# Optimization experiments

Hardware: AMD Instinct MI355X
Metric: run time of the kernel (lower is better)

## Reference

```python
import jax, jax.numpy as jnp
import numpy as np

FEAT_DIM = 1024
NUM_HEAD = 8


def setup_inputs() -> dict:
    key = jax.random.key(0)
    ks = jax.random.split(key, 8)
    D = FEAT_DIM
    s = D ** -0.5
    return {
        "motion": jax.random.normal(ks[0], (8, 1024, D), dtype=jnp.float32),
        "scene_feats": jax.random.normal(ks[1], (8, 2048, D), dtype=jnp.float32),
        # nn.Linear weights stored as [in, out] (already transposed for x @ W)
        "Wq": jax.random.normal(ks[2], (D, D), dtype=jnp.float32) * s,
        "bq": jax.random.normal(ks[3], (D,), dtype=jnp.float32) * s,
        "Wkv": jax.random.normal(ks[4], (D, 2 * D), dtype=jnp.float32) * s,
        "bkv": jax.random.normal(ks[5], (2 * D,), dtype=jnp.float32) * s,
        "Wout": jax.random.normal(ks[6], (D, D), dtype=jnp.float32) * s,
        "bout": jax.random.normal(ks[7], (D,), dtype=jnp.float32) * s,
    }


def reference(motion, scene_feats, Wq, bq, Wkv, bkv, Wout, bout):
    bs, L, D = motion.shape
    N = scene_feats.shape[1]
    H = NUM_HEAD
    Dh = D // H

    # q scaled by full feat_dim**-0.5 (as in source, not head_dim)
    q = (motion @ Wq + bq) * (D ** -0.5)
    kv = scene_feats @ Wkv + bkv
    k, v = kv[..., :D], kv[..., D:]

    # Faithful to source: q is viewed as (bs, H, L, Dh) with NO transpose,
    # while k, v use view(bs, N, H, Dh) followed by transpose(1, 2).
    q = q.reshape(bs, H, L, Dh)                      # [bs,H,L,Dh] (layout quirk)
    k = k.reshape(bs, N, H, Dh).transpose(0, 2, 1, 3)  # [bs,H,N,Dh]
    v = v.reshape(bs, N, H, Dh).transpose(0, 2, 1, 3)  # [bs,H,N,Dh]

    att = jnp.einsum("bhld,bhnd->bhln", q, k)        # [bs,H,L,N]
    att = jax.nn.softmax(att, axis=-1)
    out = jnp.einsum("bhln,bhnd->bhld", att, v)      # [bs,H,L,Dh]
    out = out.reshape(bs, L, D)                      # contiguous view, matches torch .view
    return out @ Wout + bout
```

## Files before the change

kernel.cpp:

```cpp
#include <hip/hip_runtime.h>

typedef __attribute__((ext_vector_type(8))) short bf16x8;
typedef __attribute__((ext_vector_type(4))) float f32x4;
typedef __attribute__((ext_vector_type(4))) float f32x4v;

#define MFMA16(a,b,c) __builtin_amdgcn_mfma_f32_16x16x32_bf16((a),(b),(c),0,0,0)

__device__ __forceinline__ short f2bf(float f){
  unsigned u = __builtin_bit_cast(unsigned, f);
  u += 0x7fffu + ((u >> 16) & 1u);
  return (short)(u >> 16);
}

__device__ __forceinline__ void gload16(const void* g, void* l){
  __builtin_amdgcn_global_load_lds((const __attribute__((address_space(1))) unsigned*)g,
                                   (__attribute__((address_space(3))) unsigned*)l,
                                   16, 0, 0);
}

__global__ __launch_bounds__(256) void k_f2bf(const float* __restrict__ in,
                                              short* __restrict__ out, int n8){
  int i = blockIdx.x * 256 + threadIdx.x;
  if (i >= n8) return;
  f32x4v a = ((const f32x4v*)in)[i*2];
  f32x4v b = ((const f32x4v*)in)[i*2+1];
  bf16x8 o;
  o[0]=f2bf(a[0]); o[1]=f2bf(a[1]); o[2]=f2bf(a[2]); o[3]=f2bf(a[3]);
  o[4]=f2bf(b[0]); o[5]=f2bf(b[1]); o[6]=f2bf(b[2]); o[7]=f2bf(b[3]);
  ((bf16x8*)out)[i] = o;
}

__global__ __launch_bounds__(256) void k_prep_wT(const float* __restrict__ W,
                                                 short* __restrict__ Wt, int K, int N){
  int i = blockIdx.x * 256 + threadIdx.x;
  int total = (K >> 3) * N;
  if (i >= total) return;
  int n  = i % N;
  int k0 = (i / N) << 3;
  bf16x8 o;
#pragma unroll
  for (int j = 0; j < 8; ++j) o[j] = f2bf(W[(size_t)(k0 + j) * N + n]);
  *(bf16x8*)&Wt[(size_t)n * K + k0] = o;
}

template<int MODE>
__global__ __launch_bounds__(256, 4) void k_gemm(
    const short* __restrict__ A, const short* __restrict__ Bt,
    const float* __restrict__ bias, float scale,
    void* __restrict__ out0, void* __restrict__ out1,
    int M, int N, int K)
{
  __shared__ __align__(16) short Alds[2][128 * 32];
  __shared__ __align__(16) short Blds[2][128 * 32];
  const int tid = threadIdx.x;
  const int l = tid & 63, w = tid >> 6;
  const int m0 = blockIdx.y * 128, n0 = blockIdx.x * 128;
  const int wr = w >> 1, wc = w & 1;
  const int lr = l & 15, lg = l >> 4;

  const int srow = l >> 2;
  const int scol = 8 * ((l & 3) ^ (srow & 3));
  const int acol = 8 * (lg ^ (lr & 3));

  f32x4 acc[4][4];
#pragma unroll
  for (int a = 0; a < 4; ++a)
#pragma unroll
    for (int b = 0; b < 4; ++b) acc[a][b] = (f32x4)(0.0f);

  const int nk = K >> 5;
  auto stage = [&](int kt, int buf){
    int k0 = kt << 5;
#pragma unroll
    for (int i = 0; i < 4; ++i){
      int c = w * 4 + i;
      if (c < 8){
        int m = c * 16 + srow;
        gload16(A + (size_t)(m0 + m) * K + k0 + scol, &Alds[buf][c * 512]);
      } else {
        int n = (c - 8) * 16 + srow;
        gload16(Bt + (size_t)(n0 + n) * K + k0 + scol, &Blds[buf][(c - 8) * 512]);
      }
    }
  };

  stage(0, 0);
  __syncthreads();
  int cur = 0;
  for (int kt = 0; kt < nk; ++kt){
    if (kt + 1 < nk) stage(kt + 1, cur ^ 1);
    bf16x8 af[4], bfv[4];
#pragma unroll
    for (int mi = 0; mi < 4; ++mi){
      int row = wr * 64 + mi * 16 + lr;
      af[mi] = *(const bf16x8*)&Alds[cur][row * 32 + acol];
    }
#pragma unroll
    for (int ni = 0; ni < 4; ++ni){
      int row = wc * 64 + ni * 16 + lr;
      bfv[ni] = *(const bf16x8*)&Blds[cur][row * 32 + acol];
    }
#pragma unroll
    for (int mi = 0; mi < 4; ++mi)
#pragma unroll
      for (int ni = 0; ni < 4; ++ni)
        acc[mi][ni] = MFMA16(af[mi], bfv[ni], acc[mi][ni]);
    __syncthreads();
    cur ^= 1;
  }

#pragma unroll
  for (int mi = 0; mi < 4; ++mi)
#pragma unroll
    for (int ni = 0; ni < 4; ++ni){
      int col = n0 + wc * 64 + ni * 16 + lr;
      float bv = bias[col];
#pragma unroll
      for (int r = 0; r < 4; ++r){
        int row = m0 + wr * 64 + mi * 16 + lg * 4 + r;
        float v = acc[mi][ni][r] + bv;
        if (MODE == 0){
          v *= scale;
          int b = row >> 10, lp = row & 1023;
          int h = lp >> 7;
          int lq = ((lp & 127) << 3) | (col >> 7);
          int dh = col & 127;
          ((short*)out0)[(((size_t)(b * 8 + h)) * 1024 + lq) * 128 + dh] = f2bf(v);
        } else if (MODE == 1){
          int b = row >> 11, nn = row & 2047;
          if (col < 1024){
            int h = col >> 7, dh = col & 127;
            ((short*)out0)[(((size_t)(b * 8 + h)) * 2048 + nn) * 128 + dh] = f2bf(v);
          } else {
            int c2 = col - 1024, h = c2 >> 7, dh = c2 & 127;
            ((short*)out1)[(((size_t)(b * 8 + h)) * 128 + dh) * 2048 + nn] = f2bf(v);
          }
        } else {
          ((float*)out0)[(size_t)row * N + col] = v;
        }
      }
    }
}

__global__ __launch_bounds__(512, 2) void k_attn(
    const short* __restrict__ Q, const short* __restrict__ K,
    const short* __restrict__ Vt, short* __restrict__ O)
{
  __shared__ __align__(16) short Klds[2][64 * 128];
  __shared__ __align__(16) short Vlds[2][128 * 64];
  __shared__ __align__(16) short Plds[8][32 * 64];
  const int tid = threadIdx.x;
  const int l = tid & 63, w = tid >> 6;
  const int lr = l & 15, lg = l >> 4;

  int flat = blockIdx.y * 4 + blockIdx.x;
  int xcd = flat & 7, idx = flat >> 3;
  int bh = xcd * 8 + (idx >> 2);
  int q0 = (idx & 3) * 256;

  const short* Qb = Q  + (size_t)bh * 1024 * 128;
  const short* Kb = K  + (size_t)bh * 2048 * 128;
  const short* Vb = Vt + (size_t)bh * 128 * 2048;

  bf16x8 qf[2][4];
#pragma unroll
  for (int mi = 0; mi < 2; ++mi)
#pragma unroll
    for (int kc = 0; kc < 4; ++kc)
      qf[mi][kc] = *(const bf16x8*)&Qb[(size_t)(q0 + w * 32 + mi * 16 + lr) * 128 + kc * 32 + lg * 8];

  f32x4 acc[8][2];
#pragma unroll
  for (int d = 0; d < 8; ++d){ acc[d][0] = (f32x4)(0.0f); acc[d][1] = (f32x4)(0.0f); }
  float mrun[2][4], lsum[2][4];
#pragma unroll
  for (int mi = 0; mi < 2; ++mi)
#pragma unroll
    for (int r = 0; r < 4; ++r){ mrun[mi][r] = -3e38f; lsum[mi][r] = 0.f; }

  auto stageK = [&](int t, int buf){
    int kv0 = t * 64;
#pragma unroll
    for (int i = 0; i < 2; ++i){
      int c = w * 2 + i;
      int row = 4 * c + (l >> 4);
      int col = ((l & 15) * 8) ^ ((row & 7) * 8);
      gload16(Kb + (size_t)(kv0 + row) * 128 + col, &Klds[buf][c * 512]);
    }
  };
  auto stageV = [&](int t, int buf){
    int kv0 = t * 64;
#pragma unroll
    for (int i = 0; i < 2; ++i){
      int c = w * 2 + i;
      int dh = 8 * c + (l >> 3);
      int col = ((l & 7) * 8) ^ (((l >> 3) & 7) * 8);
      gload16(Vb + (size_t)dh * 2048 + kv0 + col, &Vlds[buf][c * 512]);
    }
  };

  stageK(0, 0); stageV(0, 0);
  __syncthreads();
  int cur = 0;
  const int swz = (lr & 7) * 8;

  for (int t = 0; t < 32; ++t){
    if (t + 1 < 32){ stageK(t + 1, cur ^ 1); stageV(t + 1, cur ^ 1); }
    const short* Kl = &Klds[cur][0];
    const short* Vl = &Vlds[cur][0];
    short* Pw = &Plds[w][0];

    f32x4 s[2][4];
    __builtin_amdgcn_s_setprio(1);
#pragma unroll
    for (int nt = 0; nt < 4; ++nt){
      f32x4 s0 = (f32x4)(0.0f), s1 = (f32x4)(0.0f);
#pragma unroll
      for (int kc = 0; kc < 4; ++kc){
        bf16x8 kf = *(const bf16x8*)&Kl[(nt * 16 + lr) * 128 + ((kc * 32 + lg * 8) ^ swz)];
        s0 = MFMA16(qf[0][kc], kf, s0);
        s1 = MFMA16(qf[1][kc], kf, s1);
      }
      s[0][nt] = s0; s[1][nt] = s1;
    }
    __builtin_amdgcn_s_setprio(0);

    float pmax[2][4];
    int ok = 1;
#pragma unroll
    for (int mi = 0; mi < 2; ++mi)
#pragma unroll
      for (int r = 0; r < 4; ++r){
        float v = fmaxf(fmaxf(s[mi][0][r], s[mi][1][r]), fmaxf(s[mi][2][r], s[mi][3][r]));
        pmax[mi][r] = v;
        ok &= (v <= mrun[mi][r] + 8.0f) ? 1 : 0;
      }
    if (!__all(ok)){
#pragma unroll
      for (int mi = 0; mi < 2; ++mi)
#pragma unroll
        for (int r = 0; r < 4; ++r){
          float v = pmax[mi][r];
          v = fmaxf(v, __shfl_xor(v, 1, 16));
          v = fmaxf(v, __shfl_xor(v, 2, 16));
          v = fmaxf(v, __shfl_xor(v, 4, 16));
          v = fmaxf(v, __shfl_xor(v, 8, 16));
          float mnew = fmaxf(mrun[mi][r], v);
          float sc = exp2f(mrun[mi][r] - mnew);
          mrun[mi][r] = mnew;
          lsum[mi][r] *= sc;
#pragma unroll
          for (int d = 0; d < 8; ++d) acc[d][mi][r] *= sc;
        }
    }

#pragma unroll
    for (int mi = 0; mi < 2; ++mi)
#pragma unroll
      for (int r = 0; r < 4; ++r){
        int row = mi * 16 + lg * 4 + r;
        int rsw = (row & 7) * 8;
        float ls = 0.f;
#pragma unroll
        for (int nt = 0; nt < 4; ++nt){
          float p = exp2f(s[mi][nt][r] - mrun[mi][r]);
          ls += p;
          Pw[row * 64 + ((nt * 16 + lr) ^ rsw)] = f2bf(p);
        }
        lsum[mi][r] += ls;
      }

    bf16x8 pa[2][2];
#pragma unroll
    for (int mi = 0; mi < 2; ++mi)
#pragma unroll
      for (int kc = 0; kc < 2; ++kc)
        pa[mi][kc] = *(const bf16x8*)&Pw[(mi * 16 + lr) * 64 + ((kc * 32 + lg * 8) ^ swz)];
    __builtin_amdgcn_s_setprio(1);
#pragma unroll
    for (int d = 0; d < 8; ++d)
#pragma unroll
      for (int kc = 0; kc < 2; ++kc){
        bf16x8 vf = *(const bf16x8*)&Vl[(d * 16 + lr) * 64 + ((kc * 32 + lg * 8) ^ swz)];
        acc[d][0] = MFMA16(pa[0][kc], vf, acc[d][0]);
        acc[d][1] = MFMA16(pa[1][kc], vf, acc[d][1]);
      }
    __builtin_amdgcn_s_setprio(0);

    __syncthreads();
    cur ^= 1;
  }

  const int b = bh >> 3, h = bh & 7;
#pragma unroll
  for (int mi = 0; mi < 2; ++mi)
#pragma unroll
    for (int r = 0; r < 4; ++r){
      float ls = lsum[mi][r];
      ls += __shfl_xor(ls, 1, 16);
      ls += __shfl_xor(ls, 2, 16);
      ls += __shfl_xor(ls, 4, 16);
      ls += __shfl_xor(ls, 8, 16);
      float inv = 1.0f / ls;
      int grow = q0 + w * 32 + mi * 16 + lg * 4 + r;
      size_t base = ((size_t)b * 1024 + (size_t)h * 128 + (grow >> 3)) * 1024
                  + (size_t)(grow & 7) * 128;
#pragma unroll
      for (int d = 0; d < 8; ++d)
        O[base + d * 16 + lr] = f2bf(acc[d][mi][r] * inv);
    }
}

extern "C" void kernel_launch(void* const* d_in, const int* in_sizes, int n_in,
                              void* d_out, int out_size, void* d_ws, size_t ws_size,
                              hipStream_t stream){
  const float* motion = (const float*)d_in[0];
  const float* scene  = (const float*)d_in[1];
  const float* Wq     = (const float*)d_in[2];
  const float* bq     = (const float*)d_in[3];
  const float* Wkv    = (const float*)d_in[4];
  const float* bkv    = (const float*)d_in[5];
  const float* Wout   = (const float*)d_in[6];
  const float* bout   = (const float*)d_in[7];
  float* out = (float*)d_out;

  char* ws = (char*)d_ws;
  const size_t MB = 1024 * 1024;
  short* WqT   = (short*)(ws + 0);
  short* WkvT  = (short*)(ws + 2  * MB);
  short* WoutT = (short*)(ws + 6  * MB);
  short* mA    = (short*)(ws + 8  * MB);
  short* sA    = (short*)(ws + 24 * MB);
  short* Qb    = (short*)(ws + 56 * MB);
  short* Kb    = (short*)(ws + 72 * MB);
  short* Vtb   = (short*)(ws + 104* MB);
  short* attnO = mA;

  const float qscale = 0.03125f * 1.44269504088896341f;

  k_prep_wT<<<dim3(512),  256, 0, stream>>>(Wq,   WqT,   1024, 1024);
  k_prep_wT<<<dim3(1024), 256, 0, stream>>>(Wkv,  WkvT,  1024, 2048);
  k_prep_wT<<<dim3(512),  256, 0, stream>>>(Wout, WoutT, 1024, 1024);
  k_f2bf<<<dim3(4096), 256, 0, stream>>>(motion, mA, 1024 * 1024);
  k_f2bf<<<dim3(8192), 256, 0, stream>>>(scene,  sA, 2 * 1024 * 1024);

  k_gemm<0><<<dim3(8, 64),   256, 0, stream>>>(mA, WqT,  bq,  qscale, Qb, nullptr, 8192, 1024, 1024);
  k_gemm<1><<<dim3(16, 128), 256, 0, stream>>>(sA, WkvT, bkv, 1.0f,   Kb, Vtb,    16384, 2048, 1024);
  k_attn<<<dim3(4, 64), 512, 0, stream>>>(Qb, Kb, Vtb, attnO);
  k_gemm<2><<<dim3(8, 64), 256, 0, stream>>>(attnO, WoutT, bout, 1.0f, out, nullptr, 8192, 1024, 1024);
}
```

Baseline: 335.0 us.

## Triple-buffer LDS with one barrier per iteration, remap GEMM tiles per XCD

Both the GEMM and attention kernels go from double to triple LDS buffering and prefetch two tiles ahead. The two __syncthreads per iteration become a single s_waitcnt vmcnt(4) plus barrier, so more global-load latency overlaps with MFMA work. The GEMM also remaps block indices so consecutive tiles share an XCD for L2 reuse, and changes the LDS swizzle pattern. In exchange, LDS use grows, which may cut occupancy in the attention kernel (two 512-thread blocks requested). The tail iterations redundantly reload the last tile to keep the vmcnt accounting constant.

```diff
diff --git a/kernel.cpp b/kernel.cpp
--- a/kernel.cpp
+++ b/kernel.cpp
@@ -50,17 +50,22 @@
     void* __restrict__ out0, void* __restrict__ out1,
     int M, int N, int K)
 {
-  __shared__ __align__(16) short Alds[2][128 * 32];
-  __shared__ __align__(16) short Blds[2][128 * 32];
+  __shared__ __align__(16) short Alds[3][128 * 32];
+  __shared__ __align__(16) short Blds[3][128 * 32];
   const int tid = threadIdx.x;
   const int l = tid & 63, w = tid >> 6;
-  const int m0 = blockIdx.y * 128, n0 = blockIdx.x * 128;
   const int wr = w >> 1, wc = w & 1;
   const int lr = l & 15, lg = l >> 4;
 
+  const int nx = gridDim.x;
+  const int nwg = nx * gridDim.y;
+  int flat = blockIdx.y * nx + blockIdx.x;
+  int u = (flat & 7) * (nwg >> 3) + (flat >> 3);
+  const int m0 = (u / nx) * 128, n0 = (u % nx) * 128;
+
   const int srow = l >> 2;
-  const int scol = 8 * ((l & 3) ^ (srow & 3));
-  const int acol = 8 * (lg ^ (lr & 3));
+  const int scol = 8 * ((l & 3) ^ ((l >> 3) & 3));
+  const int acol = 8 * (lg ^ ((lr >> 1) & 3));
 
   f32x4 acc[4][4];
 #pragma unroll
@@ -69,45 +74,52 @@
     for (int b = 0; b < 4; ++b) acc[a][b] = (f32x4)(0.0f);
 
   const int nk = K >> 5;
-  auto stage = [&](int kt, int buf){
+  auto stage = [&](int kt, int slot){
     int k0 = kt << 5;
 #pragma unroll
     for (int i = 0; i < 4; ++i){
       int c = w * 4 + i;
       if (c < 8){
         int m = c * 16 + srow;
-        gload16(A + (size_t)(m0 + m) * K + k0 + scol, &Alds[buf][c * 512]);
+        gload16(A + (size_t)(m0 + m) * K + k0 + scol, &Alds[slot][c * 512]);
       } else {
         int n = (c - 8) * 16 + srow;
-        gload16(Bt + (size_t)(n0 + n) * K + k0 + scol, &Blds[buf][(c - 8) * 512]);
+        gload16(Bt + (size_t)(n0 + n) * K + k0 + scol, &Blds[slot][(c - 8) * 512]);
       }
     }
   };
 
   stage(0, 0);
-  __syncthreads();
-  int cur = 0;
+  stage(1, 1);
+  int rd = 0;
   for (int kt = 0; kt < nk; ++kt){
-    if (kt + 1 < nk) stage(kt + 1, cur ^ 1);
+    asm volatile("s_waitcnt vmcnt(4)" ::: "memory");
+    __builtin_amdgcn_s_barrier();
+    __builtin_amdgcn_sched_barrier(0);
+    int tt = (kt + 2 < nk) ? kt + 2 : nk - 1;
+    int tgt = rd + 2; if (tgt >= 3) tgt -= 3;
+    stage(tt, tgt);
+
     bf16x8 af[4], bfv[4];
 #pragma unroll
     for (int mi = 0; mi < 4; ++mi){
       int row = wr * 64 + mi * 16 + lr;
-      af[mi] = *(const bf16x8*)&Alds[cur][row * 32 + acol];
+      af[mi] = *(const bf16x8*)&Alds[rd][row * 32 + acol];
     }
 #pragma unroll
     for (int ni = 0; ni < 4; ++ni){
       int row = wc * 64 + ni * 16 + lr;
-      bfv[ni] = *(const bf16x8*)&Blds[cur][row * 32 + acol];
+      bfv[ni] = *(const bf16x8*)&Blds[rd][row * 32 + acol];
     }
 #pragma unroll
     for (int mi = 0; mi < 4; ++mi)
 #pragma unroll
       for (int ni = 0; ni < 4; ++ni)
         acc[mi][ni] = MFMA16(af[mi], bfv[ni], acc[mi][ni]);
-    __syncthreads();
-    cur ^= 1;
+
+    if (++rd == 3) rd = 0;
   }
+  asm volatile("s_waitcnt vmcnt(0)" ::: "memory");
 
 #pragma unroll
   for (int mi = 0; mi < 4; ++mi)
@@ -146,8 +158,8 @@
     const short* __restrict__ Q, const short* __restrict__ K,
     const short* __restrict__ Vt, short* __restrict__ O)
 {
-  __shared__ __align__(16) short Klds[2][64 * 128];
-  __shared__ __align__(16) short Vlds[2][128 * 64];
+  __shared__ __align__(16) short Klds[3][64 * 128];
+  __shared__ __align__(16) short Vlds[3][128 * 64];
   __shared__ __align__(16) short Plds[8][32 * 64];
   const int tid = threadIdx.x;
   const int l = tid & 63, w = tid >> 6;
@@ -178,7 +190,7 @@
 #pragma unroll
     for (int r = 0; r < 4; ++r){ mrun[mi][r] = -3e38f; lsum[mi][r] = 0.f; }
 
-  auto stageK = [&](int t, int buf){
+  auto stageKV = [&](int t, int buf){
     int kv0 = t * 64;
 #pragma unroll
     for (int i = 0; i < 2; ++i){
@@ -187,9 +199,6 @@
       int col = ((l & 15) * 8) ^ ((row & 7) * 8);
       gload16(Kb + (size_t)(kv0 + row) * 128 + col, &Klds[buf][c * 512]);
     }
-  };
-  auto stageV = [&](int t, int buf){
-    int kv0 = t * 64;
 #pragma unroll
     for (int i = 0; i < 2; ++i){
       int c = w * 2 + i;
@@ -199,15 +208,21 @@
     }
   };
 
-  stageK(0, 0); stageV(0, 0);
-  __syncthreads();
-  int cur = 0;
+  stageKV(0, 0);
+  stageKV(1, 1);
   const int swz = (lr & 7) * 8;
+  int rd = 0;
 
   for (int t = 0; t < 32; ++t){
-    if (t + 1 < 32){ stageK(t + 1, cur ^ 1); stageV(t + 1, cur ^ 1); }
-    const short* Kl = &Klds[cur][0];
-    const short* Vl = &Vlds[cur][0];
+    asm volatile("s_waitcnt vmcnt(4)" ::: "memory");
+    __builtin_amdgcn_s_barrier();
+    __builtin_amdgcn_sched_barrier(0);
+    int tt = (t + 2 < 32) ? t + 2 : 31;
+    int tgt = rd + 2; if (tgt >= 3) tgt -= 3;
+    stageKV(tt, tgt);
+
+    const short* Kl = &Klds[rd][0];
+    const short* Vl = &Vlds[rd][0];
     short* Pw = &Plds[w][0];
 
     f32x4 s[2][4];
@@ -287,9 +302,9 @@
       }
     __builtin_amdgcn_s_setprio(0);
 
-    __syncthreads();
-    cur ^= 1;
+    if (++rd == 3) rd = 0;
   }
+  asm volatile("s_waitcnt vmcnt(0)" ::: "memory");
 
   const int b = bh >> 3, h = bh & 7;
 #pragma unroll
```

After: 312.5 us. 6.7% less time.

## Deepen GEMM LDS pipeline to four stages with swizzled tile order

Applied to the files above, without the earlier changes.

The projection GEMM moves from a double-buffered LDS scheme with two barriers per k-step to a four-slot ring that prefetches three tiles ahead, using vmcnt waits and a single barrier per iteration. It also remaps workgroup IDs so that consecutive blocks spread across XCDs, and changes the LDS XOR swizzle to cut bank conflicts. LDS use doubles to 64KB per block, which may lower occupancy below the launch-bounds target of 4. The prefetch clamps to the last tile and issues redundant loads near the end of the k loop.

```diff
diff --git a/kernel.cpp b/kernel.cpp
--- a/kernel.cpp
+++ b/kernel.cpp
@@ -50,17 +50,22 @@
     void* __restrict__ out0, void* __restrict__ out1,
     int M, int N, int K)
 {
-  __shared__ __align__(16) short Alds[2][128 * 32];
-  __shared__ __align__(16) short Blds[2][128 * 32];
+  __shared__ __align__(16) short Alds[4][128 * 32];
+  __shared__ __align__(16) short Blds[4][128 * 32];
   const int tid = threadIdx.x;
   const int l = tid & 63, w = tid >> 6;
-  const int m0 = blockIdx.y * 128, n0 = blockIdx.x * 128;
   const int wr = w >> 1, wc = w & 1;
   const int lr = l & 15, lg = l >> 4;
 
+  const int nx = gridDim.x;
+  const int nwg = nx * gridDim.y;
+  int flat = blockIdx.y * nx + blockIdx.x;
+  int u = (flat & 7) * (nwg >> 3) + (flat >> 3);
+  const int m0 = (u / nx) * 128, n0 = (u % nx) * 128;
+
   const int srow = l >> 2;
-  const int scol = 8 * ((l & 3) ^ (srow & 3));
-  const int acol = 8 * (lg ^ (lr & 3));
+  const int scol = 8 * ((l & 3) ^ ((l >> 3) & 3));
+  const int acol = 8 * (lg ^ ((lr >> 1) & 3));
 
   f32x4 acc[4][4];
 #pragma unroll
@@ -69,45 +74,52 @@
     for (int b = 0; b < 4; ++b) acc[a][b] = (f32x4)(0.0f);
 
   const int nk = K >> 5;
-  auto stage = [&](int kt, int buf){
+  auto stage = [&](int kt, int slot){
     int k0 = kt << 5;
 #pragma unroll
     for (int i = 0; i < 4; ++i){
       int c = w * 4 + i;
       if (c < 8){
         int m = c * 16 + srow;
-        gload16(A + (size_t)(m0 + m) * K + k0 + scol, &Alds[buf][c * 512]);
+        gload16(A + (size_t)(m0 + m) * K + k0 + scol, &Alds[slot][c * 512]);
       } else {
         int n = (c - 8) * 16 + srow;
-        gload16(Bt + (size_t)(n0 + n) * K + k0 + scol, &Blds[buf][(c - 8) * 512]);
+        gload16(Bt + (size_t)(n0 + n) * K + k0 + scol, &Blds[slot][(c - 8) * 512]);
       }
     }
   };
 
   stage(0, 0);
-  __syncthreads();
-  int cur = 0;
+  stage(1, 1);
+  stage(2, 2);
+  int rd = 0;
   for (int kt = 0; kt < nk; ++kt){
-    if (kt + 1 < nk) stage(kt + 1, cur ^ 1);
+    asm volatile("s_waitcnt vmcnt(8)" ::: "memory");
+    __builtin_amdgcn_s_barrier();
+    int tt = (kt + 3 < nk) ? kt + 3 : nk - 1;
+    int tgt = (rd + 3) & 3;
+    stage(tt, tgt);
+
     bf16x8 af[4], bfv[4];
 #pragma unroll
     for (int mi = 0; mi < 4; ++mi){
       int row = wr * 64 + mi * 16 + lr;
-      af[mi] = *(const bf16x8*)&Alds[cur][row * 32 + acol];
+      af[mi] = *(const bf16x8*)&Alds[rd][row * 32 + acol];
     }
 #pragma unroll
     for (int ni = 0; ni < 4; ++ni){
       int row = wc * 64 + ni * 16 + lr;
-      bfv[ni] = *(const bf16x8*)&Blds[cur][row * 32 + acol];
+      bfv[ni] = *(const bf16x8*)&Blds[rd][row * 32 + acol];
     }
 #pragma unroll
     for (int mi = 0; mi < 4; ++mi)
 #pragma unroll
       for (int ni = 0; ni < 4; ++ni)
         acc[mi][ni] = MFMA16(af[mi], bfv[ni], acc[mi][ni]);
-    __syncthreads();
-    cur ^= 1;
+
+    rd = (rd + 1) & 3;
   }
+  asm volatile("s_waitcnt vmcnt(0)" ::: "memory");
 
 #pragma unroll
   for (int mi = 0; mi < 4; ++mi)
```

New measurement: 313.8 us. -6.3%, faster.
